# Optimization experiments

Hardware: AMD Instinct MI355X
Metric: run time of the kernel (lower is better)

Reference implementation:

```python
import jax, jax.numpy as jnp
import numpy as np

NUM_NODES = 8192
MUL = 64
ENV_P = 6
EPSILON = 1.0 / np.sqrt(17.0)  # 1/sqrt(1 + avg_num_neighbors), avg_num_neighbors=16


def _envelope(u, p=ENV_P):
    # polynomial smoothing envelope (cutoff at u = 1)
    a = -(p + 1) * (p + 2) / 2.0
    b = p * (p + 2)
    c = -p * (p + 1) / 2.0
    f = 1.0 + a * u ** p + b * u ** (p + 1) + c * u ** (p + 2)
    return jnp.where(u < 1.0, f, 0.0)


def setup_inputs() -> dict:
    key = jax.random.key(0)
    ks = jax.random.split(key, 9)
    E, F = 131072, 512
    vectors = jax.random.normal(ks[0], (E, 3), jnp.float32) * 0.35  # mostly inside cutoff
    x = jax.random.normal(ks[1], (E, F), jnp.float32)
    V = jax.random.normal(ks[2], (E, MUL, 4), jnp.float32)  # per mul-channel: [0e | 1o(3)]
    senders = jax.random.randint(ks[3], (E,), 0, NUM_NODES, jnp.int32)
    W_w = jax.random.normal(ks[4], (F, MUL), jnp.float32)
    W1 = jax.random.normal(ks[5], (F + 2 * MUL, 512), jnp.float32)
    W2 = jax.random.normal(ks[6], (512, 512), jnp.float32)
    W3 = jax.random.normal(ks[7], (512, 512), jnp.float32)
    W_lin = jax.random.normal(ks[8], (3 * MUL, MUL), jnp.float32)
    return {"vectors": vectors, "x": x, "V": V, "senders": senders,
            "W_w": W_w, "W1": W1, "W2": W2, "W3": W3, "W_lin": W_lin}


def reference(vectors, x, V, senders, W_w, W1, W2, W3, W_lin):
    E = vectors.shape[0]
    # edge-wise linear producing tensor-product weights  [E, MUL]
    w = (x @ W_w) / np.sqrt(x.shape[-1])
    # spherical harmonics (component norm), l = 0..1 of normalized vectors -> [E, 4]
    r = jnp.linalg.norm(vectors, axis=-1, keepdims=True)          # [E, 1]
    nhat = vectors / r
    Y = jnp.concatenate([jnp.ones((E, 1), vectors.dtype), np.sqrt(3.0) * nhat], axis=1)
    # weighted SH, scatter-sum over senders, gather back (map_back=True), scale by epsilon
    wY_e = w[:, :, None] * Y[:, None, :]                          # [E, MUL, 4]
    agg = jax.ops.segment_sum(wY_e, senders, num_segments=NUM_NODES)
    wY = agg[senders] * EPSILON                                   # [E, MUL, 4]
    # CG tensor product wY (0e+1o) x V (0e+1o), keep 0e and 1o outputs
    a0, a1 = wY[..., 0], wY[..., 1:]
    b0, b1 = V[..., 0], V[..., 1:]
    scal = jnp.concatenate(
        [a0 * b0, jnp.einsum('emi,emi->em', a1, b1) / np.sqrt(3.0)], axis=-1)  # [E, 2*MUL]
    vecs = jnp.concatenate(
        [a0[..., None] * b1, a1 * b0[..., None], jnp.cross(a1, b1) / np.sqrt(2.0)],
        axis=1)                                                   # [E, 3*MUL, 3]
    # concat scalar channel into invariants, 3-layer MLP (silu, linear last)
    xc = jnp.concatenate([x, scal], axis=1)                       # [E, 640]
    h = jax.nn.silu(xc @ W1 / np.sqrt(xc.shape[-1]))
    h = jax.nn.silu(h @ W2 / np.sqrt(h.shape[-1]))
    h = h @ W3 / np.sqrt(h.shape[-1])
    x_out = _envelope(r) * h                                      # [E, 512]
    # equivariant linear over the 1o multiplicity axis
    V_out = jnp.einsum('ekc,km->emc', vecs, W_lin) / np.sqrt(vecs.shape[1])  # [E, MUL, 3]
    return x_out, V_out
```

## Files before the change

kernel.cpp:

```cpp
#include <hip/hip_runtime.h>
#include <cstdint>
#include <cstddef>

#define E_TOT 131072
#define NNODES 8192

typedef __attribute__((ext_vector_type(8))) short bf16x8;
typedef __attribute__((ext_vector_type(4))) float f32x4;
typedef unsigned short u16;
typedef unsigned int u32;

__device__ __forceinline__ u16 f2bf(float f) {
    u32 u = __builtin_bit_cast(u32, f);
    u32 r = (u + 0x7FFFu + ((u >> 16) & 1u)) >> 16;
    return (u16)r;
}

__device__ __forceinline__ void gload16(const u16* g, u16* l) {
    __builtin_amdgcn_global_load_lds((const __attribute__((address_space(1))) void*)g,
                                     (__attribute__((address_space(3))) void*)l, 16, 0, 0);
}

__device__ __forceinline__ bf16x8 lds_frag(const u16* base, int row, int bytecol) {
    return *(const bf16x8*)((const char*)base + row * 128 + (bytecol ^ ((row & 7) << 4)));
}

__global__ void wconv_kernel(const float* __restrict__ src, u16* __restrict__ dst,
                             int K, int N) {
    int idx = blockIdx.x * 256 + threadIdx.x;
    if (idx >= N * K) return;
    int n = idx / K, k = idx - n * K;
    dst[idx] = f2bf(src[(size_t)k * N + n]);
}

__global__ void envy_kernel(const float* __restrict__ vectors, float* __restrict__ env,
                            float4* __restrict__ Y) {
    int e = blockIdx.x * 256 + threadIdx.x;
    float vx = vectors[3 * e + 0], vy = vectors[3 * e + 1], vz = vectors[3 * e + 2];
    float r2 = vx * vx + vy * vy + vz * vz;
    float r = sqrtf(r2);
    float u6 = r2 * r2 * r2;
    float f = 1.0f + u6 * (-28.0f + 48.0f * r - 21.0f * r2);
    env[e] = (r < 1.0f) ? f : 0.0f;
    float inv = 1.7320508075688772f / r;
    Y[e] = make_float4(1.0f, vx * inv, vy * inv, vz * inv);
}

__global__ void hist_kernel(const int* __restrict__ senders, int* __restrict__ cnt) {
    int e = blockIdx.x * 256 + threadIdx.x;
    atomicAdd(&cnt[senders[e]], 1);
}

__launch_bounds__(1024)
__global__ void scan_kernel(const int* __restrict__ cnt, int* __restrict__ off,
                            int* __restrict__ curs) {
    __shared__ int part[1024];
    const int t = threadIdx.x;
    int local[8];
    int s = 0;
#pragma unroll
    for (int j = 0; j < 8; ++j) { local[j] = cnt[t * 8 + j]; s += local[j]; }
    part[t] = s;
    __syncthreads();
    for (int d = 1; d < 1024; d <<= 1) {
        int v = (t >= d) ? part[t - d] : 0;
        __syncthreads();
        part[t] += v;
        __syncthreads();
    }
    int run = part[t] - s;
#pragma unroll
    for (int j = 0; j < 8; ++j) {
        off[t * 8 + j] = run;
        curs[t * 8 + j] = run;
        run += local[j];
    }
    if (t == 1023) off[8192] = run;
}

__global__ void permbuild_kernel(const int* __restrict__ senders, int* __restrict__ curs,
                                 int* __restrict__ perm) {
    int e = blockIdx.x * 256 + threadIdx.x;
    int s = senders[e];
    int p = atomicAdd(&curs[s], 1);
    perm[p] = e;
}

__launch_bounds__(256)
__global__ void gather_kernel(const float* __restrict__ w, const float4* __restrict__ Y,
                              const int* __restrict__ off, const int* __restrict__ perm,
                              float4* __restrict__ agg) {
    const int t = threadIdx.x;
    const int n = blockIdx.x * 4 + (t >> 6);
    const int m = t & 63;
    const int beg = off[n], end = off[n + 1];
    float4 acc = make_float4(0.f, 0.f, 0.f, 0.f);
    for (int i = beg; i < end; ++i) {
        int e = perm[i];
        float wv = w[(size_t)e * 64 + m];
        float4 y = Y[e];
        acc.x += wv * y.x; acc.y += wv * y.y; acc.z += wv * y.z; acc.w += wv * y.w;
    }
    agg[(size_t)n * 64 + m] = acc;
}

__launch_bounds__(256)
__global__ void wgemm_kernel(const float* __restrict__ x, const u16* __restrict__ Wt,
                             u16* __restrict__ XB, float* __restrict__ w) {
    __shared__ u16 As[128 * 72];
    __shared__ u16 Bs[64 * 72];
    const int e0 = blockIdx.x * 128;
    const int t = threadIdx.x, lane = t & 63, wid = t >> 6;
    const int lr = lane & 15, lh = lane >> 4;
    const int r8 = t >> 3, c8 = t & 7;
    f32x4 acc[2][4] = {};
    for (int kt = 0; kt < 8; ++kt) {
        const int kk = kt << 6;
#pragma unroll
        for (int i = 0; i < 4; ++i) {
            int row = i * 32 + r8;
            const float* gx = x + (size_t)(e0 + row) * 512 + kk + c8 * 8;
            float4 a = *(const float4*)gx;
            float4 b = *(const float4*)(gx + 4);
            union { u16 h[8]; uint4 v; } p;
            p.h[0] = f2bf(a.x); p.h[1] = f2bf(a.y); p.h[2] = f2bf(a.z); p.h[3] = f2bf(a.w);
            p.h[4] = f2bf(b.x); p.h[5] = f2bf(b.y); p.h[6] = f2bf(b.z); p.h[7] = f2bf(b.w);
            *(uint4*)((char*)As + row * 144 + c8 * 16) = p.v;
            *(uint4*)(XB + (size_t)(e0 + row) * 512 + kk + c8 * 8) = p.v;
        }
#pragma unroll
        for (int i = 0; i < 2; ++i) {
            int row = i * 32 + r8;
            const u16* g = Wt + (size_t)row * 512 + kk + c8 * 8;
            *(uint4*)((char*)Bs + row * 144 + c8 * 16) = *(const uint4*)g;
        }
        __syncthreads();
#pragma unroll
        for (int k2 = 0; k2 < 2; ++k2) {
            bf16x8 af[2], bfr[4];
#pragma unroll
            for (int m = 0; m < 2; ++m)
                af[m] = *(const bf16x8*)((const char*)As + (wid * 32 + m * 16 + lr) * 144 + k2 * 64 + lh * 16);
#pragma unroll
            for (int n = 0; n < 4; ++n)
                bfr[n] = *(const bf16x8*)((const char*)Bs + (n * 16 + lr) * 144 + k2 * 64 + lh * 16);
#pragma unroll
            for (int m = 0; m < 2; ++m)
#pragma unroll
                for (int n = 0; n < 4; ++n)
                    acc[m][n] = __builtin_amdgcn_mfma_f32_16x16x32_bf16(af[m], bfr[n], acc[m][n], 0, 0, 0);
        }
        __syncthreads();
    }
    const float s = 0.044194173824159216f;
#pragma unroll
    for (int m = 0; m < 2; ++m)
#pragma unroll
        for (int n = 0; n < 4; ++n)
#pragma unroll
            for (int j = 0; j < 4; ++j) {
                int e = e0 + wid * 32 + m * 16 + lh * 4 + j;
                w[(size_t)e * 64 + n * 16 + lr] = acc[m][n][j] * s;
            }
}

__launch_bounds__(256)
__global__ void edge_kernel(const int* __restrict__ senders, const float4* __restrict__ agg4,
                            const float4* __restrict__ V4, const u16* __restrict__ Wlt,
                            u16* __restrict__ scal, float* __restrict__ Vout) {
    __shared__ u16 a_lds[3][32][200];
    __shared__ u16 w_lds[64 * 200];
    const int t = threadIdx.x;
    const int e0 = blockIdx.x * 32;
#pragma unroll
    for (int i = 0; i < 6; ++i) {
        int c = i * 256 + t;
        int row = c / 24, off = (c % 24) * 8;
        *(uint4*)((char*)w_lds + row * 400 + off * 2) = ((const uint4*)Wlt)[c];
    }
    const float invs3 = 0.5773502691896258f;
    const float invs2 = 0.7071067811865476f;
    const float EPS = 0.24253562503633297f;
#pragma unroll
    for (int i = 0; i < 8; ++i) {
        int el = i * 4 + (t >> 6);
        int m = t & 63;
        int e = e0 + el;
        int s = senders[e];
        float4 a = agg4[(size_t)s * 64 + m];
        a.x *= EPS; a.y *= EPS; a.z *= EPS; a.w *= EPS;
        float4 b = V4[(size_t)e * 64 + m];
        float s0 = a.x * b.x;
        float s1 = (a.y * b.y + a.z * b.z + a.w * b.w) * invs3;
        scal[(size_t)e * 128 + m] = f2bf(s0);
        scal[(size_t)e * 128 + 64 + m] = f2bf(s1);
        float cx = (a.z * b.w - a.w * b.z) * invs2;
        float cy = (a.w * b.y - a.y * b.w) * invs2;
        float cz = (a.y * b.z - a.z * b.y) * invs2;
        a_lds[0][el][m] = f2bf(a.x * b.y);
        a_lds[0][el][64 + m] = f2bf(a.y * b.x);
        a_lds[0][el][128 + m] = f2bf(cx);
        a_lds[1][el][m] = f2bf(a.x * b.z);
        a_lds[1][el][64 + m] = f2bf(a.z * b.x);
        a_lds[1][el][128 + m] = f2bf(cy);
        a_lds[2][el][m] = f2bf(a.x * b.w);
        a_lds[2][el][64 + m] = f2bf(a.w * b.x);
        a_lds[2][el][128 + m] = f2bf(cz);
    }
    __syncthreads();
    const int lane = t & 63, wid = t >> 6;
    const int lr = lane & 15, lh = lane >> 4;
    f32x4 acc[3][2] = {};
    for (int kt = 0; kt < 6; ++kt) {
        bf16x8 bfr = *(const bf16x8*)((const char*)w_lds + (wid * 16 + lr) * 400 + kt * 64 + lh * 16);
#pragma unroll
        for (int c = 0; c < 3; ++c)
#pragma unroll
            for (int m = 0; m < 2; ++m) {
                bf16x8 afr = *(const bf16x8*)((const char*)a_lds + ((c * 32 + m * 16 + lr) * 400) + kt * 64 + lh * 16);
                acc[c][m] = __builtin_amdgcn_mfma_f32_16x16x32_bf16(afr, bfr, acc[c][m], 0, 0, 0);
            }
    }
    __syncthreads();
    float* ot = (float*)a_lds;
    const float sc = 0.07216878364870323f;
#pragma unroll
    for (int c = 0; c < 3; ++c)
#pragma unroll
        for (int m = 0; m < 2; ++m)
#pragma unroll
            for (int j = 0; j < 4; ++j) {
                int row = m * 16 + lh * 4 + j;
                int mul = wid * 16 + lr;
                ot[row * 192 + mul * 3 + c] = acc[c][m][j] * sc;
            }
    __syncthreads();
    float4* vo = (float4*)(Vout + (size_t)e0 * 192);
#pragma unroll
    for (int i = 0; i < 6; ++i)
        vo[i * 256 + t] = ((float4*)ot)[i * 256 + t];
}

template <int MODE, int K>
__launch_bounds__(512, 2)
__global__ void mlp_gemm(const u16* __restrict__ A, const u16* __restrict__ A2,
                         const u16* __restrict__ Bt, const float scale,
                         const float* __restrict__ env,
                         u16* __restrict__ outb, float* __restrict__ outf) {
    constexpr int NKT = K >> 6;
    constexpr int NSTEP = NKT * 4;
    __shared__ u16 lds[2][2][256 * 64];
    const int b = blockIdx.x;
    const int t = threadIdx.x, lane = t & 63, wid = t >> 6;
    const int wm = wid >> 2, wn = wid & 3;
    const int lr = lane & 15, lh = lane >> 4;
    const int sr8 = lane >> 3;
    const int scol = ((lane & 7) ^ sr8) << 3;
    f32x4 acc[8][4] = {};

    auto issue = [&](int g) {
        const int tile = g / NKT;
        const int kt = g - tile * NKT;
        const int tid = b * 4 + tile;
        const int e0 = (tid >> 1) << 8;
        const int n0 = (tid & 1) << 8;
        const int kk = kt << 6;
        const int col = kk + scol;
        const int buf = g & 1;
#pragma unroll
        for (int i = 0; i < 4; ++i) {
            const int row = e0 + i * 64 + wid * 8 + sr8;
            const u16* gp;
            if (A2 && kk >= 512) gp = A2 + (size_t)row * 128 + (col - 512);
            else                 gp = A + (size_t)row * 512 + col;
            gload16(gp, (u16*)&lds[buf][0][i * 4096 + wid * 512]);
        }
#pragma unroll
        for (int i = 0; i < 4; ++i) {
            const int row = n0 + i * 64 + wid * 8 + sr8;
            gload16(Bt + (size_t)row * K + col, (u16*)&lds[buf][1][i * 4096 + wid * 512]);
        }
    };

    issue(0);
    issue(1);
    for (int g = 0; g < NSTEP; ++g) {
        const int tile = g / NKT;
        const int kt = g - tile * NKT;
        if (g + 1 >= NSTEP)           asm volatile("s_waitcnt vmcnt(0)\ns_barrier" ::: "memory");
        else if (kt <= 1 && tile > 0) asm volatile("s_waitcnt vmcnt(40)\ns_barrier" ::: "memory");
        else                          asm volatile("s_waitcnt vmcnt(8)\ns_barrier" ::: "memory");
        const u16* Ab = lds[g & 1][0];
        const u16* Bb = lds[g & 1][1];
        __builtin_amdgcn_s_setprio(1);
#pragma unroll
        for (int k2 = 0; k2 < 2; ++k2) {
            bf16x8 af[8], bfr[4];
#pragma unroll
            for (int m = 0; m < 8; ++m)
                af[m] = lds_frag(Ab, wm * 128 + m * 16 + lr, k2 * 64 + lh * 16);
#pragma unroll
            for (int n = 0; n < 4; ++n)
                bfr[n] = lds_frag(Bb, wn * 64 + n * 16 + lr, k2 * 64 + lh * 16);
#pragma unroll
            for (int m = 0; m < 8; ++m)
#pragma unroll
                for (int n = 0; n < 4; ++n)
                    acc[m][n] = __builtin_amdgcn_mfma_f32_16x16x32_bf16(af[m], bfr[n], acc[m][n], 0, 0, 0);
        }
        __builtin_amdgcn_s_setprio(0);
        asm volatile("s_waitcnt lgkmcnt(0)\ns_barrier" ::: "memory");
        if (g + 2 < NSTEP) issue(g + 2);
        if (kt == NKT - 1) {
            const int tid = b * 4 + tile;
            const int e0 = (tid >> 1) << 8;
            const int n0 = (tid & 1) << 8;
#pragma unroll
            for (int m = 0; m < 8; ++m) {
#pragma unroll
                for (int j = 0; j < 4; ++j) {
                    const int row = e0 + wm * 128 + m * 16 + lh * 4 + j;
                    float ev = (MODE == 1) ? env[row] : 0.0f;
#pragma unroll
                    for (int n = 0; n < 4; ++n) {
                        const int col = n0 + wn * 64 + n * 16 + lr;
                        float v = acc[m][n][j] * scale;
                        if (MODE == 0) {
                            float sv = v / (1.0f + __expf(-v));
                            outb[(size_t)row * 512 + col] = f2bf(sv);
                        } else {
                            outf[(size_t)row * 512 + col] = v * ev;
                        }
                    }
                }
            }
#pragma unroll
            for (int m = 0; m < 8; ++m)
#pragma unroll
                for (int n = 0; n < 4; ++n)
                    acc[m][n] = f32x4{0.f, 0.f, 0.f, 0.f};
        }
    }
}

extern "C" void kernel_launch(void* const* d_in, const int* in_sizes, int n_in,
                              void* d_out, int out_size, void* d_ws, size_t ws_size,
                              hipStream_t stream) {
    const float* vectors = (const float*)d_in[0];
    const float* x       = (const float*)d_in[1];
    const float* V       = (const float*)d_in[2];
    const int*   senders = (const int*)d_in[3];
    const float* W_w     = (const float*)d_in[4];
    const float* W1      = (const float*)d_in[5];
    const float* W2      = (const float*)d_in[6];
    const float* W3      = (const float*)d_in[7];
    const float* W_lin   = (const float*)d_in[8];
    float* out = (float*)d_out;
    char* ws = (char*)d_ws;

    u16*    XB   = (u16*)(ws + 0x0);
    u16*    H1   = (u16*)(ws + 0x8000000);
    u16*    SCAL = (u16*)(ws + 0x10000000);
    float*  AGG  = (float*)(ws + 0x12000000);
    float*  ENV  = (float*)(ws + 0x12800000);
    float4* Yb   = (float4*)(ws + 0x12880000);
    float*  Wbuf = (float*)(ws + 0x12A80000);
    u16*    WT   = (u16*)(ws + 0x14A80000);
    u16* Wwt = WT;
    u16* W1t = Wwt + 64 * 512;
    u16* W2t = W1t + 512 * 640;
    u16* W3t = W2t + 512 * 512;
    u16* Wlt = W3t + 512 * 512;
    u16* H2 = XB;
    int* COUNT = (int*)(ws + 0x15000000);
    int* OFF   = (int*)(ws + 0x15010000);
    int* CURS  = (int*)(ws + 0x15020000);
    int* PERM  = (int*)(ws + 0x15030000);

    hipMemsetAsync(COUNT, 0, NNODES * sizeof(int), stream);

    wconv_kernel<<<(64 * 512) / 256, 256, 0, stream>>>(W_w, Wwt, 512, 64);
    wconv_kernel<<<(512 * 640) / 256, 256, 0, stream>>>(W1, W1t, 640, 512);
    wconv_kernel<<<(512 * 512) / 256, 256, 0, stream>>>(W2, W2t, 512, 512);
    wconv_kernel<<<(512 * 512) / 256, 256, 0, stream>>>(W3, W3t, 512, 512);
    wconv_kernel<<<(64 * 192) / 256, 256, 0, stream>>>(W_lin, Wlt, 192, 64);

    envy_kernel<<<E_TOT / 256, 256, 0, stream>>>(vectors, ENV, Yb);

    hist_kernel<<<E_TOT / 256, 256, 0, stream>>>(senders, COUNT);
    scan_kernel<<<1, 1024, 0, stream>>>(COUNT, OFF, CURS);
    permbuild_kernel<<<E_TOT / 256, 256, 0, stream>>>(senders, CURS, PERM);

    wgemm_kernel<<<E_TOT / 128, 256, 0, stream>>>(x, Wwt, XB, Wbuf);
    gather_kernel<<<NNODES / 4, 256, 0, stream>>>(Wbuf, Yb, OFF, PERM, (float4*)AGG);

    edge_kernel<<<E_TOT / 32, 256, 0, stream>>>(senders, (const float4*)AGG, (const float4*)V,
                                                Wlt, SCAL, out + (size_t)E_TOT * 512);

    const float s640 = 0.03952847075210474f;
    const float s512 = 0.044194173824159216f;
    mlp_gemm<0, 640><<<256, 512, 0, stream>>>(XB, SCAL, W1t, s640, nullptr, H1, nullptr);
    mlp_gemm<0, 512><<<256, 512, 0, stream>>>(H1, nullptr, W2t, s512, nullptr, H2, nullptr);
    mlp_gemm<1, 512><<<256, 512, 0, stream>>>(H2, nullptr, W3t, s512, ENV, nullptr, out);
}
```

Baseline: 586.5 us.

## Retile MLP GEMMs to 128x512 blocks with 32x32 MFMA and LDS-staged epilogue

The MLP GEMMs change from persistent 256-block kernels looping over four 256x256 tiles to one block per 128-row by 512-column tile, launched as E/128 blocks. The inner loop now uses 32x32x16 bf16 MFMA instead of 16x16x32. The epilogue stages accumulators through swizzled LDS so that outputs are written as 16-byte vector stores. The aim is to reuse each A tile across all 512 output columns, raise MFMA efficiency and coalesce the output writes. The cost is more B (weight) traffic per block and a larger LDS footprint of about 160KB, which with launch_bounds(512,2) may limit occupancy.

```diff
diff --git a/kernel.cpp b/kernel.cpp
--- a/kernel.cpp
+++ b/kernel.cpp
@@ -7,6 +7,7 @@
 
 typedef __attribute__((ext_vector_type(8))) short bf16x8;
 typedef __attribute__((ext_vector_type(4))) float f32x4;
+typedef __attribute__((ext_vector_type(16))) float f32x16;
 typedef unsigned short u16;
 typedef unsigned int u32;
 
@@ -248,97 +249,117 @@
                          const float* __restrict__ env,
                          u16* __restrict__ outb, float* __restrict__ outf) {
     constexpr int NKT = K >> 6;
-    constexpr int NSTEP = NKT * 4;
-    __shared__ u16 lds[2][2][256 * 64];
-    const int b = blockIdx.x;
+    __shared__ u16 lds[81920];
+    const int e0 = blockIdx.x << 7;
     const int t = threadIdx.x, lane = t & 63, wid = t >> 6;
     const int wm = wid >> 2, wn = wid & 3;
-    const int lr = lane & 15, lh = lane >> 4;
-    const int sr8 = lane >> 3;
-    const int scol = ((lane & 7) ^ sr8) << 3;
-    f32x4 acc[8][4] = {};
+    const int l31 = lane & 31, hi = lane >> 5;
+    const int srow = t >> 3;
+    const int sc8 = t & 7;
+    const int scol = ((sc8 ^ (srow & 7)) << 3);
+    f32x16 acc[2][4] = {};
+
+    auto ldsA = [&](int b) { return lds + b * 8192; };
+    auto ldsB = [&](int b) { return lds + 16384 + b * 32768; };
 
     auto issue = [&](int g) {
-        const int tile = g / NKT;
-        const int kt = g - tile * NKT;
-        const int tid = b * 4 + tile;
-        const int e0 = (tid >> 1) << 8;
-        const int n0 = (tid & 1) << 8;
-        const int kk = kt << 6;
-        const int col = kk + scol;
+        const int kk = g << 6;
         const int buf = g & 1;
 #pragma unroll
-        for (int i = 0; i < 4; ++i) {
-            const int row = e0 + i * 64 + wid * 8 + sr8;
+        for (int i = 0; i < 2; ++i) {
+            const int row = i * 64 + srow;
             const u16* gp;
-            if (A2 && kk >= 512) gp = A2 + (size_t)row * 128 + (col - 512);
-            else                 gp = A + (size_t)row * 512 + col;
-            gload16(gp, (u16*)&lds[buf][0][i * 4096 + wid * 512]);
-        }
-#pragma unroll
-        for (int i = 0; i < 4; ++i) {
-            const int row = n0 + i * 64 + wid * 8 + sr8;
-            gload16(Bt + (size_t)row * K + col, (u16*)&lds[buf][1][i * 4096 + wid * 512]);
+            if (A2 && kk >= 512) gp = A2 + (size_t)(e0 + row) * 128 + (kk - 512) + scol;
+            else                 gp = A + (size_t)(e0 + row) * 512 + kk + scol;
+            gload16(gp, ldsA(buf) + row * 64 + sc8 * 8);
+        }
+#pragma unroll
+        for (int i = 0; i < 8; ++i) {
+            const int row = i * 64 + srow;
+            gload16(Bt + (size_t)row * K + kk + scol, ldsB(buf) + row * 64 + sc8 * 8);
         }
     };
 
     issue(0);
     issue(1);
-    for (int g = 0; g < NSTEP; ++g) {
-        const int tile = g / NKT;
-        const int kt = g - tile * NKT;
-        if (g + 1 >= NSTEP)           asm volatile("s_waitcnt vmcnt(0)\ns_barrier" ::: "memory");
-        else if (kt <= 1 && tile > 0) asm volatile("s_waitcnt vmcnt(40)\ns_barrier" ::: "memory");
-        else                          asm volatile("s_waitcnt vmcnt(8)\ns_barrier" ::: "memory");
-        const u16* Ab = lds[g & 1][0];
-        const u16* Bb = lds[g & 1][1];
+    for (int g = 0; g < NKT; ++g) {
+        if (g + 1 < NKT) asm volatile("s_waitcnt vmcnt(10)\ns_barrier" ::: "memory");
+        else             asm volatile("s_waitcnt vmcnt(0)\ns_barrier" ::: "memory");
+        const u16* Ab = ldsA(g & 1);
+        const u16* Bb = ldsB(g & 1);
         __builtin_amdgcn_s_setprio(1);
 #pragma unroll
-        for (int k2 = 0; k2 < 2; ++k2) {
-            bf16x8 af[8], bfr[4];
-#pragma unroll
-            for (int m = 0; m < 8; ++m)
-                af[m] = lds_frag(Ab, wm * 128 + m * 16 + lr, k2 * 64 + lh * 16);
-#pragma unroll
-            for (int n = 0; n < 4; ++n)
-                bfr[n] = lds_frag(Bb, wn * 64 + n * 16 + lr, k2 * 64 + lh * 16);
-#pragma unroll
-            for (int m = 0; m < 8; ++m)
-#pragma unroll
-                for (int n = 0; n < 4; ++n)
-                    acc[m][n] = __builtin_amdgcn_mfma_f32_16x16x32_bf16(af[m], bfr[n], acc[m][n], 0, 0, 0);
+        for (int kc = 0; kc < 4; ++kc) {
+            bf16x8 af[2], bfr[4];
+#pragma unroll
+            for (int mb = 0; mb < 2; ++mb)
+                af[mb] = lds_frag(Ab, wm * 64 + mb * 32 + l31, kc * 32 + hi * 16);
+#pragma unroll
+            for (int nf = 0; nf < 4; ++nf)
+                bfr[nf] = lds_frag(Bb, wn * 128 + nf * 32 + l31, kc * 32 + hi * 16);
+#pragma unroll
+            for (int mb = 0; mb < 2; ++mb)
+#pragma unroll
+                for (int nf = 0; nf < 4; ++nf)
+                    acc[mb][nf] = __builtin_amdgcn_mfma_f32_32x32x16_bf16(af[mb], bfr[nf], acc[mb][nf], 0, 0, 0);
         }
         __builtin_amdgcn_s_setprio(0);
         asm volatile("s_waitcnt lgkmcnt(0)\ns_barrier" ::: "memory");
-        if (g + 2 < NSTEP) issue(g + 2);
-        if (kt == NKT - 1) {
-            const int tid = b * 4 + tile;
-            const int e0 = (tid >> 1) << 8;
-            const int n0 = (tid & 1) << 8;
-#pragma unroll
-            for (int m = 0; m < 8; ++m) {
+        if (g + 2 < NKT) issue(g + 2);
+    }
+
+    float* ep = (float*)lds + wid * 2048;
+    float envr[8];
+    if (MODE == 1) {
+#pragma unroll
+        for (int p = 0; p < 8; ++p)
+            envr[p] = env[e0 + wm * 64 + p * 8 + (lane >> 3)];
+    }
+#pragma unroll
+    for (int nf = 0; nf < 4; ++nf) {
+#pragma unroll
+        for (int mb = 0; mb < 2; ++mb)
+#pragma unroll
+            for (int r = 0; r < 16; ++r) {
+                const int crow = (r & 3) + 8 * (r >> 2) + 4 * hi;
+                const int row64 = mb * 32 + crow;
+                const int gp = (l31 >> 2) ^ (row64 & 7);
+                ep[row64 * 32 + gp * 4 + (l31 & 3)] = acc[mb][nf][r];
+            }
+        const int colb = wn * 128 + nf * 32;
+        if (MODE == 0) {
+#pragma unroll
+            for (int p = 0; p < 4; ++p) {
+                const int rowl = p * 16 + (lane >> 2);
+                const int cq = lane & 3;
+                const int g0 = (2 * cq) ^ (rowl & 7);
+                const int g1 = (2 * cq + 1) ^ (rowl & 7);
+                f32x4 a = *(f32x4*)(ep + rowl * 32 + g0 * 4);
+                f32x4 b2 = *(f32x4*)(ep + rowl * 32 + g1 * 4);
+                union { u16 h[8]; uint4 v; } pk;
 #pragma unroll
                 for (int j = 0; j < 4; ++j) {
-                    const int row = e0 + wm * 128 + m * 16 + lh * 4 + j;
-                    float ev = (MODE == 1) ? env[row] : 0.0f;
-#pragma unroll
-                    for (int n = 0; n < 4; ++n) {
-                        const int col = n0 + wn * 64 + n * 16 + lr;
-                        float v = acc[m][n][j] * scale;
-                        if (MODE == 0) {
-                            float sv = v / (1.0f + __expf(-v));
-                            outb[(size_t)row * 512 + col] = f2bf(sv);
-                        } else {
-                            outf[(size_t)row * 512 + col] = v * ev;
-                        }
-                    }
+                    float v = a[j] * scale;
+                    pk.h[j] = f2bf(v / (1.0f + __expf(-v)));
                 }
-            }
-#pragma unroll
-            for (int m = 0; m < 8; ++m)
-#pragma unroll
-                for (int n = 0; n < 4; ++n)
-                    acc[m][n] = f32x4{0.f, 0.f, 0.f, 0.f};
+#pragma unroll
+                for (int j = 0; j < 4; ++j) {
+                    float v = b2[j] * scale;
+                    pk.h[4 + j] = f2bf(v / (1.0f + __expf(-v)));
+                }
+                *(uint4*)(outb + (size_t)(e0 + wm * 64 + rowl) * 512 + colb + cq * 8) = pk.v;
+            }
+        } else {
+#pragma unroll
+            for (int p = 0; p < 8; ++p) {
+                const int rowl = p * 8 + (lane >> 3);
+                const int c = lane & 7;
+                const int gp = c ^ (rowl & 7);
+                f32x4 v = *(f32x4*)(ep + rowl * 32 + gp * 4);
+                const float sc2 = scale * envr[p];
+                v[0] *= sc2; v[1] *= sc2; v[2] *= sc2; v[3] *= sc2;
+                *(f32x4*)(outf + (size_t)(e0 + wm * 64 + rowl) * 512 + colb + c * 4) = v;
+            }
         }
     }
 }
@@ -399,7 +420,7 @@
 
     const float s640 = 0.03952847075210474f;
     const float s512 = 0.044194173824159216f;
-    mlp_gemm<0, 640><<<256, 512, 0, stream>>>(XB, SCAL, W1t, s640, nullptr, H1, nullptr);
-    mlp_gemm<0, 512><<<256, 512, 0, stream>>>(H1, nullptr, W2t, s512, nullptr, H2, nullptr);
-    mlp_gemm<1, 512><<<256, 512, 0, stream>>>(H2, nullptr, W3t, s512, ENV, nullptr, out);
-}
+    mlp_gemm<0, 640><<<E_TOT / 128, 512, 0, stream>>>(XB, SCAL, W1t, s640, nullptr, H1, nullptr);
+    mlp_gemm<0, 512><<<E_TOT / 128, 512, 0, stream>>>(H1, nullptr, W2t, s512, nullptr, H2, nullptr);
+    mlp_gemm<1, 512><<<E_TOT / 128, 512, 0, stream>>>(H2, nullptr, W3t, s512, ENV, nullptr, out);
+}
```

Result: slower. 653.1 us (+11.4%).

## Restructure MLP GEMM to one tile per block with swizzled grid and interleaved prefetch

Applied to the files above, without the earlier changes.

The MLP GEMM kernels change from persistent blocks looping over four 256x256 output tiles to one tile per block, with the grid enlarged to 1024 blocks and a block-index swizzle that groups neighbouring tiles. The K loop is split into four phases per 64-wide step, and the next step's global-to-LDS loads are issued between fragment reads and MFMAs. The aim is better overlap of loads with compute and better L2 locality. The cost is losing cross-tile prefetch and paying more block launches and prologues.

```diff
diff --git a/kernel.cpp b/kernel.cpp
--- a/kernel.cpp
+++ b/kernel.cpp
@@ -247,98 +247,91 @@
                          const u16* __restrict__ Bt, const float scale,
                          const float* __restrict__ env,
                          u16* __restrict__ outb, float* __restrict__ outf) {
-    constexpr int NKT = K >> 6;
-    constexpr int NSTEP = NKT * 4;
-    __shared__ u16 lds[2][2][256 * 64];
-    const int b = blockIdx.x;
+    constexpr int NT = K >> 6;
+    __shared__ u16 lds[65536];
+    const int nwg = gridDim.x;
+    const int bid = blockIdx.x;
+    const int swz = (bid & 7) * (nwg >> 3) + (bid >> 3);
+    const int mt = swz >> 1, nt = swz & 1;
+    const int e0 = mt << 8, n0 = nt << 8;
     const int t = threadIdx.x, lane = t & 63, wid = t >> 6;
     const int wm = wid >> 2, wn = wid & 3;
     const int lr = lane & 15, lh = lane >> 4;
-    const int sr8 = lane >> 3;
-    const int scol = ((lane & 7) ^ sr8) << 3;
     f32x4 acc[8][4] = {};
 
-    auto issue = [&](int g) {
-        const int tile = g / NKT;
-        const int kt = g - tile * NKT;
-        const int tid = b * 4 + tile;
-        const int e0 = (tid >> 1) << 8;
-        const int n0 = (tid & 1) << 8;
-        const int kk = kt << 6;
-        const int col = kk + scol;
-        const int buf = g & 1;
-#pragma unroll
-        for (int i = 0; i < 4; ++i) {
-            const int row = e0 + i * 64 + wid * 8 + sr8;
+    auto stage = [&](int tt, int kind, int h) {
+        const int kk = tt << 6;
+        u16* dst = lds + (tt & 1) * 32768 + kind * 16384 + h * 8192;
+#pragma unroll
+        for (int i = 0; i < 2; ++i) {
+            const int c = i * 512 + t;
+            const int rowin = c >> 3;
+            const int scol = ((c & 7) ^ (rowin & 7)) << 3;
             const u16* gp;
-            if (A2 && kk >= 512) gp = A2 + (size_t)row * 128 + (col - 512);
-            else                 gp = A + (size_t)row * 512 + col;
-            gload16(gp, (u16*)&lds[buf][0][i * 4096 + wid * 512]);
-        }
-#pragma unroll
-        for (int i = 0; i < 4; ++i) {
-            const int row = n0 + i * 64 + wid * 8 + sr8;
-            gload16(Bt + (size_t)row * K + col, (u16*)&lds[buf][1][i * 4096 + wid * 512]);
+            if (kind == 0) {
+                const int row = e0 + h * 128 + rowin;
+                if (A2 && kk >= 512) gp = A2 + (size_t)row * 128 + (kk - 512) + scol;
+                else                 gp = A + (size_t)row * 512 + kk + scol;
+            } else {
+                const int row = n0 + h * 128 + rowin;
+                gp = Bt + (size_t)row * K + kk + scol;
+            }
+            gload16(gp, dst + (size_t)c * 8);
         }
     };
 
-    issue(0);
-    issue(1);
-    for (int g = 0; g < NSTEP; ++g) {
-        const int tile = g / NKT;
-        const int kt = g - tile * NKT;
-        if (g + 1 >= NSTEP)           asm volatile("s_waitcnt vmcnt(0)\ns_barrier" ::: "memory");
-        else if (kt <= 1 && tile > 0) asm volatile("s_waitcnt vmcnt(40)\ns_barrier" ::: "memory");
-        else                          asm volatile("s_waitcnt vmcnt(8)\ns_barrier" ::: "memory");
-        const u16* Ab = lds[g & 1][0];
-        const u16* Bb = lds[g & 1][1];
-        __builtin_amdgcn_s_setprio(1);
-#pragma unroll
-        for (int k2 = 0; k2 < 2; ++k2) {
-            bf16x8 af[8], bfr[4];
-#pragma unroll
-            for (int m = 0; m < 8; ++m)
-                af[m] = lds_frag(Ab, wm * 128 + m * 16 + lr, k2 * 64 + lh * 16);
-#pragma unroll
-            for (int n = 0; n < 4; ++n)
-                bfr[n] = lds_frag(Bb, wn * 64 + n * 16 + lr, k2 * 64 + lh * 16);
-#pragma unroll
-            for (int m = 0; m < 8; ++m)
-#pragma unroll
-                for (int n = 0; n < 4; ++n)
-                    acc[m][n] = __builtin_amdgcn_mfma_f32_16x16x32_bf16(af[m], bfr[n], acc[m][n], 0, 0, 0);
-        }
-        __builtin_amdgcn_s_setprio(0);
-        asm volatile("s_waitcnt lgkmcnt(0)\ns_barrier" ::: "memory");
-        if (g + 2 < NSTEP) issue(g + 2);
-        if (kt == NKT - 1) {
-            const int tid = b * 4 + tile;
-            const int e0 = (tid >> 1) << 8;
-            const int n0 = (tid & 1) << 8;
-#pragma unroll
-            for (int m = 0; m < 8; ++m) {
-#pragma unroll
-                for (int j = 0; j < 4; ++j) {
-                    const int row = e0 + wm * 128 + m * 16 + lh * 4 + j;
-                    float ev = (MODE == 1) ? env[row] : 0.0f;
-#pragma unroll
-                    for (int n = 0; n < 4; ++n) {
-                        const int col = n0 + wn * 64 + n * 16 + lr;
-                        float v = acc[m][n][j] * scale;
-                        if (MODE == 0) {
-                            float sv = v / (1.0f + __expf(-v));
-                            outb[(size_t)row * 512 + col] = f2bf(sv);
-                        } else {
-                            outf[(size_t)row * 512 + col] = v * ev;
-                        }
-                    }
+    stage(0, 0, 0); stage(0, 0, 1); stage(0, 1, 0); stage(0, 1, 1);
+
+    for (int tt = 0; tt < NT; ++tt) {
+        const u16* sl = lds + (tt & 1) * 32768;
+#pragma unroll
+        for (int p = 0; p < 4; ++p) {
+            if (p == 0) asm volatile("s_waitcnt vmcnt(0)\ns_barrier" ::: "memory");
+            const int rh = p >> 1, k2 = p & 1;
+            bf16x8 af[4], bfr[4];
+#pragma unroll
+            for (int i = 0; i < 4; ++i) {
+                const int r = wm * 128 + rh * 64 + i * 16 + lr;
+                af[i] = lds_frag(sl + (r >> 7) * 8192, r & 127, k2 * 64 + lh * 16);
+            }
+#pragma unroll
+            for (int i = 0; i < 4; ++i) {
+                const int r = wn * 64 + i * 16 + lr;
+                bfr[i] = lds_frag(sl + 16384 + (r >> 7) * 8192, r & 127, k2 * 64 + lh * 16);
+            }
+            if (tt + 1 < NT) {
+                if (p == 0) { stage(tt + 1, 0, 0); stage(tt + 1, 0, 1); }
+                else if (p == 1) { stage(tt + 1, 1, 0); stage(tt + 1, 1, 1); }
+            }
+            asm volatile("s_barrier" ::: "memory");
+            __builtin_amdgcn_s_setprio(1);
+#pragma unroll
+            for (int i = 0; i < 4; ++i)
+#pragma unroll
+                for (int nf = 0; nf < 4; ++nf)
+                    acc[rh * 4 + i][nf] = __builtin_amdgcn_mfma_f32_16x16x32_bf16(
+                        af[i], bfr[nf], acc[rh * 4 + i][nf], 0, 0, 0);
+            __builtin_amdgcn_s_setprio(0);
+        }
+    }
+
+#pragma unroll
+    for (int mb = 0; mb < 8; ++mb) {
+#pragma unroll
+        for (int j = 0; j < 4; ++j) {
+            const int row = e0 + wm * 128 + mb * 16 + lh * 4 + j;
+            float ev = (MODE == 1) ? env[row] : 0.0f;
+#pragma unroll
+            for (int nf = 0; nf < 4; ++nf) {
+                const int col = n0 + wn * 64 + nf * 16 + lr;
+                float v = acc[mb][nf][j] * scale;
+                if (MODE == 0) {
+                    float sv = v / (1.0f + __expf(-v));
+                    outb[(size_t)row * 512 + col] = f2bf(sv);
+                } else {
+                    outf[(size_t)row * 512 + col] = v * ev;
                 }
             }
-#pragma unroll
-            for (int m = 0; m < 8; ++m)
-#pragma unroll
-                for (int n = 0; n < 4; ++n)
-                    acc[m][n] = f32x4{0.f, 0.f, 0.f, 0.f};
         }
     }
 }
@@ -399,7 +392,8 @@
 
     const float s640 = 0.03952847075210474f;
     const float s512 = 0.044194173824159216f;
-    mlp_gemm<0, 640><<<256, 512, 0, stream>>>(XB, SCAL, W1t, s640, nullptr, H1, nullptr);
-    mlp_gemm<0, 512><<<256, 512, 0, stream>>>(H1, nullptr, W2t, s512, nullptr, H2, nullptr);
-    mlp_gemm<1, 512><<<256, 512, 0, stream>>>(H2, nullptr, W3t, s512, ENV, nullptr, out);
-}
+    const int gemm_grid = (E_TOT / 256) * 2;
+    mlp_gemm<0, 640><<<gemm_grid, 512, 0, stream>>>(XB, SCAL, W1t, s640, nullptr, H1, nullptr);
+    mlp_gemm<0, 512><<<gemm_grid, 512, 0, stream>>>(H1, nullptr, W2t, s512, nullptr, H2, nullptr);
+    mlp_gemm<1, 512><<<gemm_grid, 512, 0, stream>>>(H2, nullptr, W3t, s512, ENV, nullptr, out);
+}
```

Measured after the change: 611.6 us. +4.3%, slower.

## Replace persistent 256x256 multi-tile GEMM with 128x128 tiles and swizzled grid

Applied to the files above, without the earlier changes.

The MLP GEMMs move from a persistent 256-block, 512-thread kernel that walks four 256x256 output tiles per block to one 128x128 tile per 256-thread block, launched over 4096 blocks. A blockIdx swizzle groups blocks so that neighbouring ones share A and B tiles in cache. The aim is better load balance and occupancy, with a smaller LDS footprint and fewer accumulator registers per wave. The cost is lower arithmetic intensity per tile, more global and L2 traffic, and per-block launch and prologue overhead in place of cross-tile prefetch.

```diff
diff --git a/kernel.cpp b/kernel.cpp
--- a/kernel.cpp
+++ b/kernel.cpp
@@ -242,103 +242,93 @@
 }
 
 template <int MODE, int K>
-__launch_bounds__(512, 2)
+__launch_bounds__(256, 2)
 __global__ void mlp_gemm(const u16* __restrict__ A, const u16* __restrict__ A2,
                          const u16* __restrict__ Bt, const float scale,
                          const float* __restrict__ env,
                          u16* __restrict__ outb, float* __restrict__ outf) {
     constexpr int NKT = K >> 6;
-    constexpr int NSTEP = NKT * 4;
-    __shared__ u16 lds[2][2][256 * 64];
-    const int b = blockIdx.x;
+    __shared__ u16 lds[2][2][128 * 64];
+    const int nwg = gridDim.x;
+    const int bid = blockIdx.x;
+    const int swz = (bid & 7) * (nwg >> 3) + (bid >> 3);
+    const int mt = swz >> 2, nt = swz & 3;
+    const int e0 = mt << 7, n0 = nt << 7;
     const int t = threadIdx.x, lane = t & 63, wid = t >> 6;
-    const int wm = wid >> 2, wn = wid & 3;
+    const int wm = wid >> 1, wn = wid & 1;
     const int lr = lane & 15, lh = lane >> 4;
-    const int sr8 = lane >> 3;
-    const int scol = ((lane & 7) ^ sr8) << 3;
-    f32x4 acc[8][4] = {};
-
-    auto issue = [&](int g) {
-        const int tile = g / NKT;
-        const int kt = g - tile * NKT;
-        const int tid = b * 4 + tile;
-        const int e0 = (tid >> 1) << 8;
-        const int n0 = (tid & 1) << 8;
+    f32x4 acc[4][4] = {};
+
+    auto issue = [&](int kt) {
         const int kk = kt << 6;
-        const int col = kk + scol;
-        const int buf = g & 1;
+        const int buf = kt & 1;
 #pragma unroll
         for (int i = 0; i < 4; ++i) {
-            const int row = e0 + i * 64 + wid * 8 + sr8;
+            const int c = i * 256 + t;
+            const int rowin = c >> 3;
+            const int scol = ((c & 7) ^ (rowin & 7)) << 3;
             const u16* gp;
-            if (A2 && kk >= 512) gp = A2 + (size_t)row * 128 + (col - 512);
-            else                 gp = A + (size_t)row * 512 + col;
-            gload16(gp, (u16*)&lds[buf][0][i * 4096 + wid * 512]);
+            if (A2 && kk >= 512) gp = A2 + (size_t)(e0 + rowin) * 128 + (kk - 512) + scol;
+            else                 gp = A + (size_t)(e0 + rowin) * 512 + kk + scol;
+            gload16(gp, (u16*)&lds[buf][0][0] + (size_t)c * 8);
         }
 #pragma unroll
         for (int i = 0; i < 4; ++i) {
-            const int row = n0 + i * 64 + wid * 8 + sr8;
-            gload16(Bt + (size_t)row * K + col, (u16*)&lds[buf][1][i * 4096 + wid * 512]);
+            const int c = i * 256 + t;
+            const int rowin = c >> 3;
+            const int scol = ((c & 7) ^ (rowin & 7)) << 3;
+            gload16(Bt + (size_t)(n0 + rowin) * K + kk + scol,
+                    (u16*)&lds[buf][1][0] + (size_t)c * 8);
         }
     };
 
     issue(0);
     issue(1);
-    for (int g = 0; g < NSTEP; ++g) {
-        const int tile = g / NKT;
-        const int kt = g - tile * NKT;
-        if (g + 1 >= NSTEP)           asm volatile("s_waitcnt vmcnt(0)\ns_barrier" ::: "memory");
-        else if (kt <= 1 && tile > 0) asm volatile("s_waitcnt vmcnt(40)\ns_barrier" ::: "memory");
-        else                          asm volatile("s_waitcnt vmcnt(8)\ns_barrier" ::: "memory");
-        const u16* Ab = lds[g & 1][0];
-        const u16* Bb = lds[g & 1][1];
+    for (int kt = 0; kt < NKT; ++kt) {
+        if (kt + 1 < NKT) asm volatile("s_waitcnt vmcnt(8)\ns_barrier" ::: "memory");
+        else              asm volatile("s_waitcnt vmcnt(0)\ns_barrier" ::: "memory");
+        const u16* Ab = lds[kt & 1][0];
+        const u16* Bb = lds[kt & 1][1];
         __builtin_amdgcn_s_setprio(1);
 #pragma unroll
         for (int k2 = 0; k2 < 2; ++k2) {
-            bf16x8 af[8], bfr[4];
-#pragma unroll
-            for (int m = 0; m < 8; ++m)
-                af[m] = lds_frag(Ab, wm * 128 + m * 16 + lr, k2 * 64 + lh * 16);
+            bf16x8 af[4], bfr[4];
+#pragma unroll
+            for (int m = 0; m < 4; ++m)
+                af[m] = lds_frag(Ab, wm * 64 + m * 16 + lr, k2 * 64 + lh * 16);
 #pragma unroll
             for (int n = 0; n < 4; ++n)
                 bfr[n] = lds_frag(Bb, wn * 64 + n * 16 + lr, k2 * 64 + lh * 16);
 #pragma unroll
-            for (int m = 0; m < 8; ++m)
+            for (int m = 0; m < 4; ++m)
 #pragma unroll
                 for (int n = 0; n < 4; ++n)
                     acc[m][n] = __builtin_amdgcn_mfma_f32_16x16x32_bf16(af[m], bfr[n], acc[m][n], 0, 0, 0);
         }
         __builtin_amdgcn_s_setprio(0);
-        asm volatile("s_waitcnt lgkmcnt(0)\ns_barrier" ::: "memory");
-        if (g + 2 < NSTEP) issue(g + 2);
-        if (kt == NKT - 1) {
-            const int tid = b * 4 + tile;
-            const int e0 = (tid >> 1) << 8;
-            const int n0 = (tid & 1) << 8;
-#pragma unroll
-            for (int m = 0; m < 8; ++m) {
-#pragma unroll
-                for (int j = 0; j < 4; ++j) {
-                    const int row = e0 + wm * 128 + m * 16 + lh * 4 + j;
-                    float ev = (MODE == 1) ? env[row] : 0.0f;
-#pragma unroll
-                    for (int n = 0; n < 4; ++n) {
-                        const int col = n0 + wn * 64 + n * 16 + lr;
-                        float v = acc[m][n][j] * scale;
-                        if (MODE == 0) {
-                            float sv = v / (1.0f + __expf(-v));
-                            outb[(size_t)row * 512 + col] = f2bf(sv);
-                        } else {
-                            outf[(size_t)row * 512 + col] = v * ev;
-                        }
-                    }
+        if (kt + 2 < NKT) {
+            asm volatile("s_waitcnt lgkmcnt(0)\ns_barrier" ::: "memory");
+            issue(kt + 2);
+        }
+    }
+
+#pragma unroll
+    for (int m = 0; m < 4; ++m) {
+#pragma unroll
+        for (int j = 0; j < 4; ++j) {
+            const int row = e0 + wm * 64 + m * 16 + lh * 4 + j;
+            float ev = (MODE == 1) ? env[row] : 0.0f;
+#pragma unroll
+            for (int n = 0; n < 4; ++n) {
+                const int col = n0 + wn * 64 + n * 16 + lr;
+                float v = acc[m][n][j] * scale;
+                if (MODE == 0) {
+                    float sv = v / (1.0f + __expf(-v));
+                    outb[(size_t)row * 512 + col] = f2bf(sv);
+                } else {
+                    outf[(size_t)row * 512 + col] = v * ev;
                 }
             }
-#pragma unroll
-            for (int m = 0; m < 8; ++m)
-#pragma unroll
-                for (int n = 0; n < 4; ++n)
-                    acc[m][n] = f32x4{0.f, 0.f, 0.f, 0.f};
         }
     }
 }
@@ -399,7 +389,8 @@
 
     const float s640 = 0.03952847075210474f;
     const float s512 = 0.044194173824159216f;
-    mlp_gemm<0, 640><<<256, 512, 0, stream>>>(XB, SCAL, W1t, s640, nullptr, H1, nullptr);
-    mlp_gemm<0, 512><<<256, 512, 0, stream>>>(H1, nullptr, W2t, s512, nullptr, H2, nullptr);
-    mlp_gemm<1, 512><<<256, 512, 0, stream>>>(H2, nullptr, W3t, s512, ENV, nullptr, out);
-}
+    const int gemm_grid = (E_TOT / 128) * 4;
+    mlp_gemm<0, 640><<<gemm_grid, 256, 0, stream>>>(XB, SCAL, W1t, s640, nullptr, H1, nullptr);
+    mlp_gemm<0, 512><<<gemm_grid, 256, 0, stream>>>(H1, nullptr, W2t, s512, nullptr, H2, nullptr);
+    mlp_gemm<1, 512><<<gemm_grid, 256, 0, stream>>>(H2, nullptr, W3t, s512, ENV, nullptr, out);
+}
```

Measured after the change: 617.8 us. 1.05x slower.
